# Kernel tuning notes

Hardware: AMD Instinct MI355X
Metric: run time of the kernel (lower is better)

## Reference

```python
import jax, jax.numpy as jnp
import numpy as np
from jax import lax

N_T, N_CAPS, CAP_DIM = 8, 16, 16
EPS = 1e-6


def setup_inputs() -> dict:
    key = jax.random.key(0)
    k1, k2 = jax.random.split(key)
    B, H, W = 4, 64, 64
    C = N_T * N_CAPS * CAP_DIM  # 2048
    z = jax.random.normal(k1, (B, C, H, W), dtype=jnp.float32)
    u = jax.random.normal(k2, (B, C, H, W), dtype=jnp.float32)
    weight = jnp.ones((1, 1, 3, 3, 1), dtype=jnp.float32)  # Conv3d (O,I,kT,kD,kS), init ones
    beta = jnp.ones((1,), dtype=jnp.float32)  # correlated_mean_beta, mu_init=1.0
    return {"z": z, "u": u, "weight": weight, "beta": beta}


def reference(z, u, weight, beta):
    B, C, H, W = u.shape
    hw = H * W
    # (B, n_t, n_caps, cap_dim, hw) -> (B, n_caps, n_t, cap_dim, hw) -> (B*n_caps, 1, n_t, cap_dim, hw)
    u_caps = u.reshape(B, N_T, N_CAPS, CAP_DIM, hw)
    u_caps = jnp.transpose(u_caps, (0, 2, 1, 3, 4))
    u_caps = u_caps.reshape(-1, 1, N_T, CAP_DIM, hw)
    u_sq = u_caps * u_caps
    # circular pad over transform and cap_dim axes to keep 'same' size with 3x3x1 kernel
    padded = jnp.pad(u_sq, ((0, 0), (0, 0), (1, 1), (1, 1), (0, 0)), mode="wrap")
    v = lax.conv_general_dilated(
        padded, weight, window_strides=(1, 1, 1), padding="VALID",
        dimension_numbers=("NCDHW", "OIDHW", "NCDHW"),
    )  # (B*n_caps, 1, n_t, cap_dim, hw)
    v = v.reshape(B, N_CAPS, N_T, CAP_DIM, hw)
    v = jnp.transpose(v, (0, 2, 1, 3, 4)).reshape(z.shape)
    std = lax.rsqrt(v + EPS)
    s = (z + beta) * std
    return s
```

## Files before the change

### kernel.cpp

```cpp
#include <hip/hip_runtime.h>

#define N_T 8
#define N_CAPS 16
#define CAP_DIM 16
#define HW 4096
#define P_TILE 64
#define NTILES 4
#define EPS 1e-6f

__global__ __launch_bounds__(256, 2) void caps_norm_kernel(
    const float* __restrict__ z, const float* __restrict__ u,
    const float* __restrict__ w, const float* __restrict__ beta,
    float* __restrict__ out)
{
    __shared__ float lds[2][128 * P_TILE];

    const int tid = threadIdx.x;
    const int bid = blockIdx.x;
    const int pg  = bid & 15;
    const int c   = (bid >> 4) & 15;
    const int b   = bid >> 8;
    const int pbase = pg * (P_TILE * NTILES);

    float W9[9];
#pragma unroll
    for (int i = 0; i < 9; ++i) W9[i] = w[i];
    const float bet = beta[0];

    const size_t base_b = (size_t)b * 2048 * HW;

    int RR[8], QQ[8];
    size_t GOFF[8];
#pragma unroll
    for (int k = 0; k < 8; ++k) {
        int s = tid + (k << 8);
        int r = s >> 4, q = s & 15;
        int t = r >> 4, d = r & 15;
        int ch = t * 256 + c * 16 + d;
        RR[k] = r; QQ[k] = q;
        GOFF[k] = base_b + (size_t)ch * HW + (size_t)(q << 2);
    }

    float4 uN[8], zA[8], zB[8];

#define STAGE_LOAD(TI, ZREG)                                                 \
    {                                                                        \
        const int p0_ = pbase + (TI) * P_TILE;                               \
        _Pragma("unroll")                                                    \
        for (int k = 0; k < 8; ++k) {                                        \
            uN[k]   = *(const float4*)(u + GOFF[k] + p0_);                   \
            ZREG[k] = *(const float4*)(z + GOFF[k] + p0_);                   \
        }                                                                    \
    }

#define SQ_WRITE(BUF)                                                        \
    {                                                                        \
        _Pragma("unroll")                                                    \
        for (int k = 0; k < 8; ++k) {                                        \
            float4 v = uN[k];                                                \
            float4 sq;                                                       \
            sq.x = v.x*v.x; sq.y = v.y*v.y; sq.z = v.z*v.z; sq.w = v.w*v.w;  \
            *(float4*)(&lds[BUF][RR[k] * P_TILE + QQ[k] * 4]) = sq;          \
        }                                                                    \
    }

#define COMPUTE(TI, BUF, ZREG)                                               \
    {                                                                        \
        const int p0_ = pbase + (TI) * P_TILE;                               \
        _Pragma("unroll")                                                    \
        for (int k = 0; k < 8; ++k) {                                        \
            int r = RR[k], q = QQ[k];                                        \
            int t = r >> 4, d = r & 15;                                      \
            float ax = 0.f, ay = 0.f, az = 0.f, aw = 0.f;                    \
            _Pragma("unroll")                                                \
            for (int i = 0; i < 3; ++i) {                                    \
                int tt = (t + i + 7) & 7;                                    \
                _Pragma("unroll")                                            \
                for (int j = 0; j < 3; ++j) {                                \
                    int dd = (d + j + 15) & 15;                              \
                    float ww = W9[i * 3 + j];                                \
                    const float4 a = *(const float4*)(                       \
                        &lds[BUF][((tt << 4) + dd) * P_TILE + q * 4]);       \
                    ax += ww*a.x; ay += ww*a.y; az += ww*a.z; aw += ww*a.w;  \
                }                                                            \
            }                                                                \
            const float4 z4 = ZREG[k];                                       \
            float4 o;                                                        \
            o.x = (z4.x + bet) * rsqrtf(ax + EPS);                           \
            o.y = (z4.y + bet) * rsqrtf(ay + EPS);                           \
            o.z = (z4.z + bet) * rsqrtf(az + EPS);                           \
            o.w = (z4.w + bet) * rsqrtf(aw + EPS);                           \
            *(float4*)(out + GOFF[k] + p0_) = o;                             \
        }                                                                    \
    }

    STAGE_LOAD(0, zA)
    SQ_WRITE(0)
    __syncthreads();

    STAGE_LOAD(1, zB)
    COMPUTE(0, 0, zA)
    SQ_WRITE(1)
    __syncthreads();

    STAGE_LOAD(2, zA)
    COMPUTE(1, 1, zB)
    SQ_WRITE(0)
    __syncthreads();

    STAGE_LOAD(3, zB)
    COMPUTE(2, 0, zA)
    SQ_WRITE(1)
    __syncthreads();

    COMPUTE(3, 1, zB)

#undef STAGE_LOAD
#undef SQ_WRITE
#undef COMPUTE
}

extern "C" void kernel_launch(void* const* d_in, const int* in_sizes, int n_in,
                              void* d_out, int out_size, void* d_ws, size_t ws_size,
                              hipStream_t stream) {
    const float* z    = (const float*)d_in[0];
    const float* u    = (const float*)d_in[1];
    const float* w    = (const float*)d_in[2];
    const float* beta = (const float*)d_in[3];
    float* out = (float*)d_out;

    caps_norm_kernel<<<dim3(1024), dim3(256), 0, stream>>>(z, u, w, beta, out);
}
```

Before: 321.2 us.

## Enlarge pixel tile, single LDS buffer, load z at compute time

```diff
diff --git a/kernel.cpp b/kernel.cpp
--- a/kernel.cpp
+++ b/kernel.cpp
@@ -4,23 +4,23 @@
 #define N_CAPS 16
 #define CAP_DIM 16
 #define HW 4096
-#define P_TILE 64
-#define NTILES 4
+#define PT 256
+#define NT 4
 #define EPS 1e-6f
 
-__global__ __launch_bounds__(256, 2) void caps_norm_kernel(
+__global__ __launch_bounds__(512, 2) void caps_norm_kernel(
     const float* __restrict__ z, const float* __restrict__ u,
     const float* __restrict__ w, const float* __restrict__ beta,
     float* __restrict__ out)
 {
-    __shared__ float lds[2][128 * P_TILE];
+    __shared__ float lds[128 * PT];
 
     const int tid = threadIdx.x;
     const int bid = blockIdx.x;
-    const int pg  = bid & 15;
-    const int c   = (bid >> 4) & 15;
-    const int b   = bid >> 8;
-    const int pbase = pg * (P_TILE * NTILES);
+    const int pg  = bid & 3;
+    const int c   = (bid >> 2) & 15;
+    const int b   = bid >> 6;
+    const int pbase = pg * (PT * NT);
 
     float W9[9];
 #pragma unroll
@@ -28,48 +28,48 @@
     const float bet = beta[0];
 
     const size_t base_b = (size_t)b * 2048 * HW;
+    const float* ub = u + base_b;
+    const float* zb = z + base_b;
+    float*       ob = out + base_b;
 
-    int RR[8], QQ[8];
-    size_t GOFF[8];
+    const int wv = tid >> 6;
+    const int q  = tid & 63;
+
+    int OFF[16];
 #pragma unroll
-    for (int k = 0; k < 8; ++k) {
-        int s = tid + (k << 8);
-        int r = s >> 4, q = s & 15;
+    for (int k = 0; k < 16; ++k) {
+        int r = wv + (k << 3);
         int t = r >> 4, d = r & 15;
-        int ch = t * 256 + c * 16 + d;
-        RR[k] = r; QQ[k] = q;
-        GOFF[k] = base_b + (size_t)ch * HW + (size_t)(q << 2);
+        OFF[k] = (t * 256 + c * 16 + d) * HW + (q << 2);
     }
 
-    float4 uN[8], zA[8], zB[8];
+    float4 uA[16], uB[16];
 
-#define STAGE_LOAD(TI, ZREG)                                                 \
+#define STAGE_U(TI, UR)                                                      \
     {                                                                        \
-        const int p0_ = pbase + (TI) * P_TILE;                               \
+        const int p0_ = pbase + (TI) * PT;                                   \
         _Pragma("unroll")                                                    \
-        for (int k = 0; k < 8; ++k) {                                        \
-            uN[k]   = *(const float4*)(u + GOFF[k] + p0_);                   \
-            ZREG[k] = *(const float4*)(z + GOFF[k] + p0_);                   \
+        for (int k = 0; k < 16; ++k)                                         \
+            UR[k] = *(const float4*)(ub + OFF[k] + p0_);                     \
+    }
+
+#define SQW(UR)                                                              \
+    {                                                                        \
+        _Pragma("unroll")                                                    \
+        for (int k = 0; k < 16; ++k) {                                       \
+            float4 v = UR[k];                                                \
+            float4 sq;                                                       \
+            sq.x = v.x*v.x; sq.y = v.y*v.y; sq.z = v.z*v.z; sq.w = v.w*v.w;  \
+            *(float4*)(&lds[((wv + (k << 3)) << 8) + (q << 2)]) = sq;        \
         }                                                                    \
     }
 
-#define SQ_WRITE(BUF)                                                        \
+#define COMP(TI)                                                             \
     {                                                                        \
+        const int p0_ = pbase + (TI) * PT;                                   \
         _Pragma("unroll")                                                    \
-        for (int k = 0; k < 8; ++k) {                                        \
-            float4 v = uN[k];                                                \
-            float4 sq;                                                       \
-            sq.x = v.x*v.x; sq.y = v.y*v.y; sq.z = v.z*v.z; sq.w = v.w*v.w;  \
-            *(float4*)(&lds[BUF][RR[k] * P_TILE + QQ[k] * 4]) = sq;          \
-        }                                                                    \
-    }
-
-#define COMPUTE(TI, BUF, ZREG)                                               \
-    {                                                                        \
-        const int p0_ = pbase + (TI) * P_TILE;                               \
-        _Pragma("unroll")                                                    \
-        for (int k = 0; k < 8; ++k) {                                        \
-            int r = RR[k], q = QQ[k];                                        \
+        for (int k = 0; k < 16; ++k) {                                       \
+            int r = wv + (k << 3);                                           \
             int t = r >> 4, d = r & 15;                                      \
             float ax = 0.f, ay = 0.f, az = 0.f, aw = 0.f;                    \
             _Pragma("unroll")                                                \
@@ -80,44 +80,47 @@
                     int dd = (d + j + 15) & 15;                              \
                     float ww = W9[i * 3 + j];                                \
                     const float4 a = *(const float4*)(                       \
-                        &lds[BUF][((tt << 4) + dd) * P_TILE + q * 4]);       \
+                        &lds[(((tt << 4) + dd) << 8) + (q << 2)]);           \
                     ax += ww*a.x; ay += ww*a.y; az += ww*a.z; aw += ww*a.w;  \
                 }                                                            \
             }                                                                \
-            const float4 z4 = ZREG[k];                                       \
+            const float4 z4 = *(const float4*)(zb + OFF[k] + p0_);           \
             float4 o;                                                        \
             o.x = (z4.x + bet) * rsqrtf(ax + EPS);                           \
             o.y = (z4.y + bet) * rsqrtf(ay + EPS);                           \
             o.z = (z4.z + bet) * rsqrtf(az + EPS);                           \
             o.w = (z4.w + bet) * rsqrtf(aw + EPS);                           \
-            *(float4*)(out + GOFF[k] + p0_) = o;                             \
+            *(float4*)(ob + OFF[k] + p0_) = o;                               \
         }                                                                    \
     }
 
-    STAGE_LOAD(0, zA)
-    SQ_WRITE(0)
+    STAGE_U(0, uA)
+    SQW(uA)
     __syncthreads();
 
-    STAGE_LOAD(1, zB)
-    COMPUTE(0, 0, zA)
-    SQ_WRITE(1)
+    STAGE_U(1, uB)
+    COMP(0)
+    __syncthreads();
+    SQW(uB)
     __syncthreads();
 
-    STAGE_LOAD(2, zA)
-    COMPUTE(1, 1, zB)
-    SQ_WRITE(0)
+    STAGE_U(2, uA)
+    COMP(1)
+    __syncthreads();
+    SQW(uA)
     __syncthreads();
 
-    STAGE_LOAD(3, zB)
-    COMPUTE(2, 0, zA)
-    SQ_WRITE(1)
+    STAGE_U(3, uB)
+    COMP(2)
+    __syncthreads();
+    SQW(uB)
     __syncthreads();
 
-    COMPUTE(3, 1, zB)
+    COMP(3)
 
-#undef STAGE_LOAD
-#undef SQ_WRITE
-#undef COMPUTE
+#undef STAGE_U
+#undef SQW
+#undef COMP
 }
 
 extern "C" void kernel_launch(void* const* d_in, const int* in_sizes, int n_in,
@@ -129,5 +132,5 @@
     const float* beta = (const float*)d_in[3];
     float* out = (float*)d_out;
 
-    caps_norm_kernel<<<dim3(1024), dim3(256), 0, stream>>>(z, u, w, beta, out);
+    caps_norm_kernel<<<dim3(256), dim3(512), 0, stream>>>(z, u, w, beta, out);
 }
```

Result: slower. 349.1 us (+8.7%).
